# Optimization experiments

Measured on AMD Instinct MI355X. Metric: run time of the kernel, lower is better.

The kernel has to match this reference:

```python
import jax, jax.numpy as jnp
import numpy as np

D_MODEL = 512
N_HEADS = 8
D_K = D_MODEL // N_HEADS
WINDOW = 64
SCALE = 1.0 / np.sqrt(D_K)


def setup_inputs() -> dict:
    key = jax.random.key(0)
    ks = jax.random.split(key, 9)
    B, S = 1, 2048
    s = 1.0 / np.sqrt(D_MODEL)
    inp = {
        "x": jax.random.normal(ks[0], (B, S, D_MODEL), dtype=jnp.float32),
        "Wq": jax.random.normal(ks[1], (D_MODEL, D_MODEL), dtype=jnp.float32) * s,
        "bq": jnp.zeros((D_MODEL,), dtype=jnp.float32),
        "Wk": jax.random.normal(ks[2], (D_MODEL, D_MODEL), dtype=jnp.float32) * s,
        "bk": jnp.zeros((D_MODEL,), dtype=jnp.float32),
        "Wv": jax.random.normal(ks[3], (D_MODEL, D_MODEL), dtype=jnp.float32) * s,
        "bv": jnp.zeros((D_MODEL,), dtype=jnp.float32),
        "Wo": jax.random.normal(ks[4], (D_MODEL, D_MODEL), dtype=jnp.float32) * s,
        "bo": jnp.zeros((D_MODEL,), dtype=jnp.float32),
    }
    return inp


def reference(x, Wq, bq, Wk, bk, Wv, bv, Wo, bo):
    B, S, _ = x.shape
    # projections (torch Linear: x @ W.T + b); split heads -> [B,S,H,dk]
    q = (x @ Wq.T + bq).reshape(B, S, N_HEADS, D_K)
    k = (x @ Wk.T + bk).reshape(B, S, N_HEADS, D_K)
    v = (x @ Wv.T + bv).reshape(B, S, N_HEADS, D_K)

    # banded window indices: position i attends to [i-W, i+W]
    L = 2 * WINDOW + 1
    offsets = jnp.arange(L) - WINDOW                    # [L]
    pos = jnp.arange(S)[:, None] + offsets[None, :]     # [S, L]
    valid = (pos >= 0) & (pos < S)                      # [S, L]
    posc = jnp.clip(pos, 0, S - 1)

    k_w = k[:, posc]                                    # [B, S, L, H, dk]
    v_w = v[:, posc]                                    # [B, S, L, H, dk]

    scores = jnp.einsum("bshd,bslhd->bhsl", q, k_w) * SCALE
    scores = jnp.where(valid[None, None, :, :], scores, -jnp.inf)
    attn = jax.nn.softmax(scores, axis=-1)              # [B, H, S, L]
    out = jnp.einsum("bhsl,bslhd->bshd", attn, v_w)     # [B, S, H, dk]
    out = out.reshape(B, S, D_MODEL)
    return out @ Wo.T + bo
```

## Files before the change

kernel.cpp:

```cpp
#include <hip/hip_runtime.h>
#include <hip/hip_bf16.h>
#include <math.h>

#define S_LEN  2048
#define DMODEL 512
#define NHEADS 8
#define DK     64
#define WIN    64

static constexpr float SCALE = 0.125f;

typedef short bf16x8 __attribute__((ext_vector_type(8)));
typedef float f32x4  __attribute__((ext_vector_type(4)));

__device__ __forceinline__ short bfh(float v)
{
    __hip_bfloat16 b = __float2bfloat16(v);
    return *reinterpret_cast<short*>(&b);
}
__device__ __forceinline__ float bf2f(short s)
{
    __hip_bfloat16 b = *reinterpret_cast<__hip_bfloat16*>(&s);
    return __bfloat162float(b);
}
__device__ __forceinline__ void split1(float v, short& h, short& l)
{
    h = bfh(v);
    l = bfh(v - bf2f(h));
}
__device__ __forceinline__ void split8(const float4 a0, const float4 a1,
                                       bf16x8& h8, bf16x8& l8)
{
    short hh, ll;
    split1(a0.x, hh, ll); h8[0] = hh; l8[0] = ll;
    split1(a0.y, hh, ll); h8[1] = hh; l8[1] = ll;
    split1(a0.z, hh, ll); h8[2] = hh; l8[2] = ll;
    split1(a0.w, hh, ll); h8[3] = hh; l8[3] = ll;
    split1(a1.x, hh, ll); h8[4] = hh; l8[4] = ll;
    split1(a1.y, hh, ll); h8[5] = hh; l8[5] = ll;
    split1(a1.z, hh, ll); h8[6] = hh; l8[6] = ll;
    split1(a1.w, hh, ll); h8[7] = hh; l8[7] = ll;
}

__device__ __forceinline__ void dma16(const void* g, void* l)
{
    __builtin_amdgcn_global_load_lds(
        (const __attribute__((address_space(1))) unsigned int*)g,
        (__attribute__((address_space(3))) unsigned int*)l, 16, 0, 0);
}

__global__ __launch_bounds__(256)
void cast_w(const float* __restrict__ wq, const float* __restrict__ wk,
            const float* __restrict__ wv, const float* __restrict__ wo,
            short* __restrict__ wqb, short* __restrict__ wkb,
            short* __restrict__ wvb, short* __restrict__ wob)
{
    const float* s; short* d;
    switch (blockIdx.z) {
        case 0:  s = wq; d = wqb; break;
        case 1:  s = wk; d = wkb; break;
        case 2:  s = wv; d = wvb; break;
        default: s = wo; d = wob; break;
    }
    for (int i = blockIdx.x * 256 + threadIdx.x; i < 65536; i += gridDim.x * 256) {
        const float4 v = ((const float4*)s)[i];
        short4 o;
        o.x = bfh(v.x); o.y = bfh(v.y); o.z = bfh(v.z); o.w = bfh(v.w);
        ((short4*)d)[i] = o;
    }
}

__global__ __launch_bounds__(128)
void gemm_qkv4(const float* __restrict__ x,
               const short* __restrict__ wqb, const short* __restrict__ wkb,
               const short* __restrict__ wvb,
               const float* __restrict__ bq, const float* __restrict__ bk,
               const float* __restrict__ bv,
               short* __restrict__ qh, short* __restrict__ ql,
               short* __restrict__ kb, short* __restrict__ vbt)
{
    __shared__ __align__(16) short sB[64 * 256];

    const int z = blockIdx.z;
    const short* Bg   = (z == 0) ? wqb : (z == 1) ? wkb : wvb;
    const float* bias = (z == 0) ? bq  : (z == 1) ? bk  : bv;
    const int row0 = blockIdx.y * 64;
    const int col0 = blockIdx.x * 64;
    const int tid  = threadIdx.x;
    const int lane = tid & 63;
    const int wv   = tid >> 6;
    const int col  = lane & 15;
    const int quad = lane >> 4;

    f32x4 acc[2][4];
#pragma unroll
    for (int mi = 0; mi < 2; ++mi)
#pragma unroll
        for (int nj = 0; nj < 4; ++nj)
            acc[mi][nj] = (f32x4)0.0f;

    for (int ph = 0; ph < 2; ++ph) {
        __syncthreads();
        for (int i = wv; i < 32; i += 2) {
            const int q = i * 64 + lane;
            const int r = q >> 5;
            const int b = q & 31;
            const int j = b ^ (r & 7);
            dma16(Bg + (size_t)(col0 + r) * 512 + ph * 256 + j * 8, sB + i * 512);
        }
        __syncthreads();

#pragma unroll
        for (int kc = 0; kc < 8; ++kc) {
            const int k = ph * 256 + kc * 32;
            bf16x8 ah[2], al[2];
#pragma unroll
            for (int mi = 0; mi < 2; ++mi) {
                const int m = row0 + wv * 32 + mi * 16 + col;
                const float* xp = x + (size_t)m * 512 + k + quad * 8;
                const float4 a0 = *(const float4*)xp;
                const float4 a1 = *(const float4*)(xp + 4);
                split8(a0, a1, ah[mi], al[mi]);
            }
#pragma unroll
            for (int nj = 0; nj < 4; ++nj) {
                const int n = nj * 16 + col;
                const int j = (kc * 4 + quad) ^ (n & 7);
                const bf16x8 bf = *(const bf16x8*)&sB[n * 256 + j * 8];
#pragma unroll
                for (int mi = 0; mi < 2; ++mi) {
                    acc[mi][nj] = __builtin_amdgcn_mfma_f32_16x16x32_bf16(ah[mi], bf, acc[mi][nj], 0, 0, 0);
                    acc[mi][nj] = __builtin_amdgcn_mfma_f32_16x16x32_bf16(al[mi], bf, acc[mi][nj], 0, 0, 0);
                }
            }
        }
    }

#pragma unroll
    for (int nj = 0; nj < 4; ++nj) {
        const int cc = col0 + nj * 16 + col;
        const float bias_v = bias[cc];
#pragma unroll
        for (int mi = 0; mi < 2; ++mi) {
#pragma unroll
            for (int e = 0; e < 4; ++e) {
                const int row = row0 + wv * 32 + mi * 16 + quad * 4 + e;
                const float val = acc[mi][nj][e] + bias_v;
                if (z == 0) {
                    short hh, ll;
                    split1(val, hh, ll);
                    qh[(size_t)row * 512 + cc] = hh;
                    ql[(size_t)row * 512 + cc] = ll;
                } else if (z == 1) {
                    kb[(size_t)row * 512 + cc] = bfh(val);
                } else {
                    vbt[(size_t)cc * 2048 + row] = bfh(val);
                }
            }
        }
    }
}

__global__ __launch_bounds__(128)
void gemm_out4(const short* __restrict__ ah_g,
               const short* __restrict__ wob, const float* __restrict__ bo,
               float* __restrict__ out)
{
    __shared__ __align__(16) short sB[64 * 256];

    const int row0 = blockIdx.y * 32;
    const int col0 = blockIdx.x * 64;
    const int tid  = threadIdx.x;
    const int lane = tid & 63;
    const int wv   = tid >> 6;
    const int col  = lane & 15;
    const int quad = lane >> 4;

    f32x4 acc[4];
#pragma unroll
    for (int nj = 0; nj < 4; ++nj)
        acc[nj] = (f32x4)0.0f;

    for (int ph = 0; ph < 2; ++ph) {
        __syncthreads();
        for (int i = wv; i < 32; i += 2) {
            const int q = i * 64 + lane;
            const int r = q >> 5;
            const int b = q & 31;
            const int j = b ^ (r & 7);
            dma16(wob + (size_t)(col0 + r) * 512 + ph * 256 + j * 8, sB + i * 512);
        }
        __syncthreads();

#pragma unroll
        for (int kc = 0; kc < 8; ++kc) {
            const int k = ph * 256 + kc * 32;
            const int m = row0 + wv * 16 + col;
            const bf16x8 ah = *(const bf16x8*)(ah_g + (size_t)m * 512 + k + quad * 8);
#pragma unroll
            for (int nj = 0; nj < 4; ++nj) {
                const int n = nj * 16 + col;
                const int j = (kc * 4 + quad) ^ (n & 7);
                const bf16x8 bf = *(const bf16x8*)&sB[n * 256 + j * 8];
                acc[nj] = __builtin_amdgcn_mfma_f32_16x16x32_bf16(ah, bf, acc[nj], 0, 0, 0);
            }
        }
    }

#pragma unroll
    for (int nj = 0; nj < 4; ++nj) {
        const int cc = col0 + nj * 16 + col;
        const float bias_v = bo[cc];
#pragma unroll
        for (int e = 0; e < 4; ++e) {
            const int row = row0 + wv * 16 + quad * 4 + e;
            out[(size_t)row * 512 + cc] = acc[nj][e] + bias_v;
        }
    }
}

__global__ __launch_bounds__(256)
void banded_attn4(const short* __restrict__ qh, const short* __restrict__ ql,
                  const short* __restrict__ kb, const short* __restrict__ vbt,
                  short* __restrict__ abh)
{
    __shared__ __align__(16) short VtS[64 * 256];
    __shared__ __align__(16) short KS [192 * 64];
    __shared__ __align__(16) short QhS[32 * 64];
    __shared__ __align__(16) short QlS[32 * 64];
    __shared__ float pmax[4][32];
    __shared__ float psum[4][32];
    short* PS = KS;

    const int h    = blockIdx.x;
    const int t0   = blockIdx.y * 32;
    const int tid  = threadIdx.x;
    const int lane = tid & 63;
    const int wv   = tid >> 6;
    const int col  = lane & 15;
    const int quad = lane >> 4;

    {
        const int lr = lane >> 3;
        const int lc = lane & 7;
        for (int i = wv; i < 32; i += 4) {
            const short* src; short* dst; int r;
            if (i < 4) {
                r = i * 8 + lr;
                src = qh + (size_t)(t0 + r) * 512 + h * 64;
                dst = QhS + i * 512;
            } else if (i < 8) {
                const int g = i - 4;
                r = g * 8 + lr;
                src = ql + (size_t)(t0 + r) * 512 + h * 64;
                dst = QlS + g * 512;
            } else {
                const int g = i - 8;
                r = g * 8 + lr;
                int pos = t0 - 64 + r;
                pos = pos < 0 ? 0 : (pos > 2047 ? 2047 : pos);
                src = kb + (size_t)pos * 512 + h * 64;
                dst = KS + g * 512;
            }
            const int cs = lc ^ (r & 7);
            dma16(src + cs * 8, dst);
        }
        for (int i = wv; i < 32; i += 4) {
            const int q = i * 64 + lane;
            const int d = q >> 5;
            const int b = q & 31;
            const int j0 = (b < 24) ? b : 0;
            const int j = j0 ^ (d & 7);
            int p0 = t0 - 64 + j * 8;
            p0 = p0 < 0 ? 0 : (p0 > 2040 ? 2040 : p0);
            dma16(vbt + (size_t)(h * 64 + d) * 2048 + p0, VtS + i * 512);
        }
    }
    __syncthreads();

    f32x4 sacc[2][3];
#pragma unroll
    for (int mi = 0; mi < 2; ++mi)
#pragma unroll
        for (int nj = 0; nj < 3; ++nj)
            sacc[mi][nj] = (f32x4)0.0f;

#pragma unroll
    for (int ks = 0; ks < 2; ++ks) {
        const int q0 = ks * 4 + quad;
        bf16x8 aqh[2], aql[2];
#pragma unroll
        for (int mi = 0; mi < 2; ++mi) {
            const int m = mi * 16 + col;
            const int p = q0 ^ (m & 7);
            aqh[mi] = *(const bf16x8*)&QhS[m * 64 + p * 8];
            aql[mi] = *(const bf16x8*)&QlS[m * 64 + p * 8];
        }
#pragma unroll
        for (int nj = 0; nj < 3; ++nj) {
            const int n = wv * 48 + nj * 16 + col;
            const int p = q0 ^ (n & 7);
            const bf16x8 bkf = *(const bf16x8*)&KS[n * 64 + p * 8];
#pragma unroll
            for (int mi = 0; mi < 2; ++mi) {
                sacc[mi][nj] = __builtin_amdgcn_mfma_f32_16x16x32_bf16(aqh[mi], bkf, sacc[mi][nj], 0, 0, 0);
                sacc[mi][nj] = __builtin_amdgcn_mfma_f32_16x16x32_bf16(aql[mi], bkf, sacc[mi][nj], 0, 0, 0);
            }
        }
    }

    float pv[2][3][4];
#pragma unroll
    for (int mi = 0; mi < 2; ++mi)
#pragma unroll
        for (int nj = 0; nj < 3; ++nj)
#pragma unroll
            for (int e = 0; e < 4; ++e) {
                const int r32 = mi * 16 + quad * 4 + e;
                const int n   = wv * 48 + nj * 16 + col;
                const int pos = t0 - 64 + n;
                const int d   = n - r32;
                const bool valid = (pos >= 0) && (pos < S_LEN) && (d >= 0) && (d <= 128);
                pv[mi][nj][e] = valid ? sacc[mi][nj][e] * SCALE : -__builtin_inff();
            }

#pragma unroll
    for (int mi = 0; mi < 2; ++mi)
#pragma unroll
        for (int e = 0; e < 4; ++e) {
            float mx = fmaxf(fmaxf(pv[mi][0][e], pv[mi][1][e]), pv[mi][2][e]);
#pragma unroll
            for (int off = 1; off < 16; off <<= 1)
                mx = fmaxf(mx, __shfl_xor(mx, off));
            if ((lane & 15) == 0) pmax[wv][mi * 16 + quad * 4 + e] = mx;
        }
    __syncthreads();

#pragma unroll
    for (int mi = 0; mi < 2; ++mi)
#pragma unroll
        for (int e = 0; e < 4; ++e) {
            const int r32 = mi * 16 + quad * 4 + e;
            const float m = fmaxf(fmaxf(pmax[0][r32], pmax[1][r32]),
                                  fmaxf(pmax[2][r32], pmax[3][r32]));
            float ss = 0.f;
#pragma unroll
            for (int nj = 0; nj < 3; ++nj) {
                const float p = __expf(pv[mi][nj][e] - m);
                pv[mi][nj][e] = p;
                ss += p;
            }
#pragma unroll
            for (int off = 1; off < 16; off <<= 1)
                ss += __shfl_xor(ss, off);
            if ((lane & 15) == 0) psum[wv][r32] = ss;
#pragma unroll
            for (int nj = 0; nj < 3; ++nj) {
                const int n = wv * 48 + nj * 16 + col;
                PS[r32 * 200 + n] = bfh(pv[mi][nj][e]);
            }
        }
    __syncthreads();

    const int mi = wv >> 1;
    f32x4 oacc[2];
    oacc[0] = (f32x4)0.0f;
    oacc[1] = (f32x4)0.0f;
#pragma unroll
    for (int ks = 0; ks < 6; ++ks) {
        const bf16x8 pa = *(const bf16x8*)&PS[(mi * 16 + col) * 200 + ks * 32 + quad * 8];
#pragma unroll
        for (int t = 0; t < 2; ++t) {
            const int d = ((wv & 1) * 2 + t) * 16 + col;
            const int j = (ks * 4 + quad) ^ (d & 7);
            const bf16x8 vf = *(const bf16x8*)&VtS[d * 256 + j * 8];
            oacc[t] = __builtin_amdgcn_mfma_f32_16x16x32_bf16(pa, vf, oacc[t], 0, 0, 0);
        }
    }

    float linv[4];
#pragma unroll
    for (int e = 0; e < 4; ++e) {
        const int r32 = mi * 16 + quad * 4 + e;
        linv[e] = 1.0f / (psum[0][r32] + psum[1][r32] + psum[2][r32] + psum[3][r32]);
    }
#pragma unroll
    for (int t = 0; t < 2; ++t) {
        const int nj = (wv & 1) * 2 + t;
#pragma unroll
        for (int e = 0; e < 4; ++e) {
            const int r32 = mi * 16 + quad * 4 + e;
            const float val = oacc[t][e] * linv[e];
            const size_t idx = (size_t)(t0 + r32) * 512 + h * 64 + nj * 16 + col;
            abh[idx] = bfh(val);
        }
    }
}

extern "C" void kernel_launch(void* const* d_in, const int* in_sizes, int n_in,
                              void* d_out, int out_size, void* d_ws, size_t ws_size,
                              hipStream_t stream)
{
    const float* x  = (const float*)d_in[0];
    const float* Wq = (const float*)d_in[1];
    const float* bq = (const float*)d_in[2];
    const float* Wk = (const float*)d_in[3];
    const float* bk = (const float*)d_in[4];
    const float* Wv = (const float*)d_in[5];
    const float* bv = (const float*)d_in[6];
    const float* Wo = (const float*)d_in[7];
    const float* bo = (const float*)d_in[8];
    float* out = (float*)d_out;

    char* ws = (char*)d_ws;
    short* qh  = (short*)(ws);
    short* ql  = (short*)(ws + (2u << 20));
    short* kb  = (short*)(ws + (4u << 20));
    short* vbt = (short*)(ws + (6u << 20));
    short* abh = (short*)(ws + (8u << 20));
    short* wqb = (short*)(ws + (12u << 20));
    short* wkb = (short*)(ws + (12u << 20) + 1 * (512u << 10));
    short* wvb = (short*)(ws + (12u << 20) + 2 * (512u << 10));
    short* wob = (short*)(ws + (12u << 20) + 3 * (512u << 10));

    dim3 gw(64, 1, 4);
    cast_w<<<gw, 256, 0, stream>>>(Wq, Wk, Wv, Wo, wqb, wkb, wvb, wob);

    dim3 gq(DMODEL / 64, S_LEN / 64, 3);
    gemm_qkv4<<<gq, 128, 0, stream>>>(x, wqb, wkb, wvb,
                                      bq, bk, bv, qh, ql, kb, vbt);

    dim3 ga(NHEADS, S_LEN / 32);
    banded_attn4<<<ga, 256, 0, stream>>>(qh, ql, kb, vbt, abh);

    dim3 go(DMODEL / 64, S_LEN / 32);
    gemm_out4<<<go, 128, 0, stream>>>(abh, wob, bo, out);
}
```

Before: 112.5 us.

## Fuse weight bf16 conversion into projection GEMMs and drop cast kernel

Removes the separate weight-cast kernel and its extra launch. The QKV and output GEMMs now DMA fp32 weights into shared memory with an XOR swizzle and round them to bf16 in registers just before each MFMA. The QKV GEMM tile drops to 32 rows, doubling its block count, and the x hi/lo split uses a bit-trick rounding. In exchange each weight tile takes twice the LDS bytes per k-chunk and every block repeats the fp32-to-bf16 packing work.

```diff
diff --git a/kernel.cpp b/kernel.cpp
--- a/kernel.cpp
+++ b/kernel.cpp
@@ -28,18 +28,37 @@
     h = bfh(v);
     l = bfh(v - bf2f(h));
 }
-__device__ __forceinline__ void split8(const float4 a0, const float4 a1,
-                                       bf16x8& h8, bf16x8& l8)
-{
-    short hh, ll;
-    split1(a0.x, hh, ll); h8[0] = hh; l8[0] = ll;
-    split1(a0.y, hh, ll); h8[1] = hh; l8[1] = ll;
-    split1(a0.z, hh, ll); h8[2] = hh; l8[2] = ll;
-    split1(a0.w, hh, ll); h8[3] = hh; l8[3] = ll;
-    split1(a1.x, hh, ll); h8[4] = hh; l8[4] = ll;
-    split1(a1.y, hh, ll); h8[5] = hh; l8[5] = ll;
-    split1(a1.z, hh, ll); h8[6] = hh; l8[6] = ll;
-    split1(a1.w, hh, ll); h8[7] = hh; l8[7] = ll;
+
+__device__ __forceinline__ unsigned rhu2(float f0, float f1)
+{
+    unsigned b0, b1;
+    __builtin_memcpy(&b0, &f0, 4);
+    __builtin_memcpy(&b1, &f1, 4);
+    return ((b1 + 0x8000u) & 0xffff0000u) | ((b0 + 0x8000u) >> 16);
+}
+__device__ __forceinline__ bf16x8 packW(const float4 w0, const float4 w1)
+{
+    union { unsigned u[4]; bf16x8 v; } r;
+    r.u[0] = rhu2(w0.x, w0.y);
+    r.u[1] = rhu2(w0.z, w0.w);
+    r.u[2] = rhu2(w1.x, w1.y);
+    r.u[3] = rhu2(w1.z, w1.w);
+    return r.v;
+}
+__device__ __forceinline__ void splitx8(const float4 a0, const float4 a1,
+                                        bf16x8& h8, bf16x8& l8)
+{
+    float f[8] = {a0.x, a0.y, a0.z, a0.w, a1.x, a1.y, a1.z, a1.w};
+#pragma unroll
+    for (int i = 0; i < 8; ++i) {
+        unsigned b;
+        __builtin_memcpy(&b, &f[i], 4);
+        const unsigned hb = (b + 0x8000u) & 0xffff0000u;
+        h8[i] = (short)(hb >> 16);
+        float hf;
+        __builtin_memcpy(&hf, &hb, 4);
+        l8[i] = bfh(f[i] - hf);
+    }
 }
 
 __device__ __forceinline__ void dma16(const void* g, void* l)
@@ -49,125 +68,20 @@
         (__attribute__((address_space(3))) unsigned int*)l, 16, 0, 0);
 }
 
-__global__ __launch_bounds__(256)
-void cast_w(const float* __restrict__ wq, const float* __restrict__ wk,
-            const float* __restrict__ wv, const float* __restrict__ wo,
-            short* __restrict__ wqb, short* __restrict__ wkb,
-            short* __restrict__ wvb, short* __restrict__ wob)
-{
-    const float* s; short* d;
-    switch (blockIdx.z) {
-        case 0:  s = wq; d = wqb; break;
-        case 1:  s = wk; d = wkb; break;
-        case 2:  s = wv; d = wvb; break;
-        default: s = wo; d = wob; break;
-    }
-    for (int i = blockIdx.x * 256 + threadIdx.x; i < 65536; i += gridDim.x * 256) {
-        const float4 v = ((const float4*)s)[i];
-        short4 o;
-        o.x = bfh(v.x); o.y = bfh(v.y); o.z = bfh(v.z); o.w = bfh(v.w);
-        ((short4*)d)[i] = o;
-    }
-}
-
 __global__ __launch_bounds__(128)
-void gemm_qkv4(const float* __restrict__ x,
-               const short* __restrict__ wqb, const short* __restrict__ wkb,
-               const short* __restrict__ wvb,
+void gemm_qkv5(const float* __restrict__ x,
+               const float* __restrict__ Wqf, const float* __restrict__ Wkf,
+               const float* __restrict__ Wvf,
                const float* __restrict__ bq, const float* __restrict__ bk,
                const float* __restrict__ bv,
                short* __restrict__ qh, short* __restrict__ ql,
                short* __restrict__ kb, short* __restrict__ vbt)
 {
-    __shared__ __align__(16) short sB[64 * 256];
+    __shared__ __align__(16) float sW[64 * 128];
 
     const int z = blockIdx.z;
-    const short* Bg   = (z == 0) ? wqb : (z == 1) ? wkb : wvb;
+    const float* Wg   = (z == 0) ? Wqf : (z == 1) ? Wkf : Wvf;
     const float* bias = (z == 0) ? bq  : (z == 1) ? bk  : bv;
-    const int row0 = blockIdx.y * 64;
-    const int col0 = blockIdx.x * 64;
-    const int tid  = threadIdx.x;
-    const int lane = tid & 63;
-    const int wv   = tid >> 6;
-    const int col  = lane & 15;
-    const int quad = lane >> 4;
-
-    f32x4 acc[2][4];
-#pragma unroll
-    for (int mi = 0; mi < 2; ++mi)
-#pragma unroll
-        for (int nj = 0; nj < 4; ++nj)
-            acc[mi][nj] = (f32x4)0.0f;
-
-    for (int ph = 0; ph < 2; ++ph) {
-        __syncthreads();
-        for (int i = wv; i < 32; i += 2) {
-            const int q = i * 64 + lane;
-            const int r = q >> 5;
-            const int b = q & 31;
-            const int j = b ^ (r & 7);
-            dma16(Bg + (size_t)(col0 + r) * 512 + ph * 256 + j * 8, sB + i * 512);
-        }
-        __syncthreads();
-
-#pragma unroll
-        for (int kc = 0; kc < 8; ++kc) {
-            const int k = ph * 256 + kc * 32;
-            bf16x8 ah[2], al[2];
-#pragma unroll
-            for (int mi = 0; mi < 2; ++mi) {
-                const int m = row0 + wv * 32 + mi * 16 + col;
-                const float* xp = x + (size_t)m * 512 + k + quad * 8;
-                const float4 a0 = *(const float4*)xp;
-                const float4 a1 = *(const float4*)(xp + 4);
-                split8(a0, a1, ah[mi], al[mi]);
-            }
-#pragma unroll
-            for (int nj = 0; nj < 4; ++nj) {
-                const int n = nj * 16 + col;
-                const int j = (kc * 4 + quad) ^ (n & 7);
-                const bf16x8 bf = *(const bf16x8*)&sB[n * 256 + j * 8];
-#pragma unroll
-                for (int mi = 0; mi < 2; ++mi) {
-                    acc[mi][nj] = __builtin_amdgcn_mfma_f32_16x16x32_bf16(ah[mi], bf, acc[mi][nj], 0, 0, 0);
-                    acc[mi][nj] = __builtin_amdgcn_mfma_f32_16x16x32_bf16(al[mi], bf, acc[mi][nj], 0, 0, 0);
-                }
-            }
-        }
-    }
-
-#pragma unroll
-    for (int nj = 0; nj < 4; ++nj) {
-        const int cc = col0 + nj * 16 + col;
-        const float bias_v = bias[cc];
-#pragma unroll
-        for (int mi = 0; mi < 2; ++mi) {
-#pragma unroll
-            for (int e = 0; e < 4; ++e) {
-                const int row = row0 + wv * 32 + mi * 16 + quad * 4 + e;
-                const float val = acc[mi][nj][e] + bias_v;
-                if (z == 0) {
-                    short hh, ll;
-                    split1(val, hh, ll);
-                    qh[(size_t)row * 512 + cc] = hh;
-                    ql[(size_t)row * 512 + cc] = ll;
-                } else if (z == 1) {
-                    kb[(size_t)row * 512 + cc] = bfh(val);
-                } else {
-                    vbt[(size_t)cc * 2048 + row] = bfh(val);
-                }
-            }
-        }
-    }
-}
-
-__global__ __launch_bounds__(128)
-void gemm_out4(const short* __restrict__ ah_g,
-               const short* __restrict__ wob, const float* __restrict__ bo,
-               float* __restrict__ out)
-{
-    __shared__ __align__(16) short sB[64 * 256];
-
     const int row0 = blockIdx.y * 32;
     const int col0 = blockIdx.x * 64;
     const int tid  = threadIdx.x;
@@ -175,34 +89,111 @@
     const int wv   = tid >> 6;
     const int col  = lane & 15;
     const int quad = lane >> 4;
+    const int m    = row0 + wv * 16 + col;
 
     f32x4 acc[4];
 #pragma unroll
     for (int nj = 0; nj < 4; ++nj)
         acc[nj] = (f32x4)0.0f;
 
-    for (int ph = 0; ph < 2; ++ph) {
+    for (int ph = 0; ph < 4; ++ph) {
         __syncthreads();
         for (int i = wv; i < 32; i += 2) {
-            const int q = i * 64 + lane;
-            const int r = q >> 5;
-            const int b = q & 31;
-            const int j = b ^ (r & 7);
-            dma16(wob + (size_t)(col0 + r) * 512 + ph * 256 + j * 8, sB + i * 512);
+            const int r = 2 * i + (lane >> 5);
+            const int c = lane & 31;
+            const int j = c ^ (r & 7);
+            dma16(Wg + (size_t)(col0 + r) * 512 + ph * 128 + j * 4, sW + i * 256);
         }
         __syncthreads();
 
 #pragma unroll
-        for (int kc = 0; kc < 8; ++kc) {
-            const int k = ph * 256 + kc * 32;
-            const int m = row0 + wv * 16 + col;
-            const bf16x8 ah = *(const bf16x8*)(ah_g + (size_t)m * 512 + k + quad * 8);
+        for (int kc = 0; kc < 4; ++kc) {
+            const int k = ph * 128 + kc * 32;
+            const float* xp = x + (size_t)m * 512 + k + quad * 8;
+            const float4 a0 = *(const float4*)xp;
+            const float4 a1 = *(const float4*)(xp + 4);
+            bf16x8 ah, al;
+            splitx8(a0, a1, ah, al);
 #pragma unroll
             for (int nj = 0; nj < 4; ++nj) {
-                const int n = nj * 16 + col;
-                const int j = (kc * 4 + quad) ^ (n & 7);
-                const bf16x8 bf = *(const bf16x8*)&sB[n * 256 + j * 8];
-                acc[nj] = __builtin_amdgcn_mfma_f32_16x16x32_bf16(ah, bf, acc[nj], 0, 0, 0);
+                const int n  = nj * 16 + col;
+                const int s  = n & 7;
+                const int c0 = kc * 8 + quad * 2;
+                const float4 w0 = *(const float4*)&sW[n * 128 + ((c0    ) ^ s) * 4];
+                const float4 w1 = *(const float4*)&sW[n * 128 + ((c0 + 1) ^ s) * 4];
+                const bf16x8 wf = packW(w0, w1);
+                acc[nj] = __builtin_amdgcn_mfma_f32_16x16x32_bf16(ah, wf, acc[nj], 0, 0, 0);
+                acc[nj] = __builtin_amdgcn_mfma_f32_16x16x32_bf16(al, wf, acc[nj], 0, 0, 0);
+            }
+        }
+    }
+
+#pragma unroll
+    for (int nj = 0; nj < 4; ++nj) {
+        const int cc = col0 + nj * 16 + col;
+        const float bias_v = bias[cc];
+#pragma unroll
+        for (int e = 0; e < 4; ++e) {
+            const int row = row0 + wv * 16 + quad * 4 + e;
+            const float val = acc[nj][e] + bias_v;
+            if (z == 0) {
+                short hh, ll;
+                split1(val, hh, ll);
+                qh[(size_t)row * 512 + cc] = hh;
+                ql[(size_t)row * 512 + cc] = ll;
+            } else if (z == 1) {
+                kb[(size_t)row * 512 + cc] = bfh(val);
+            } else {
+                vbt[(size_t)cc * 2048 + row] = bfh(val);
+            }
+        }
+    }
+}
+
+__global__ __launch_bounds__(128)
+void gemm_out5(const short* __restrict__ ah_g,
+               const float* __restrict__ Wof, const float* __restrict__ bo,
+               float* __restrict__ out)
+{
+    __shared__ __align__(16) float sW[64 * 128];
+
+    const int row0 = blockIdx.y * 32;
+    const int col0 = blockIdx.x * 64;
+    const int tid  = threadIdx.x;
+    const int lane = tid & 63;
+    const int wv   = tid >> 6;
+    const int col  = lane & 15;
+    const int quad = lane >> 4;
+    const int m    = row0 + wv * 16 + col;
+
+    f32x4 acc[4];
+#pragma unroll
+    for (int nj = 0; nj < 4; ++nj)
+        acc[nj] = (f32x4)0.0f;
+
+    for (int ph = 0; ph < 4; ++ph) {
+        __syncthreads();
+        for (int i = wv; i < 32; i += 2) {
+            const int r = 2 * i + (lane >> 5);
+            const int c = lane & 31;
+            const int j = c ^ (r & 7);
+            dma16(Wof + (size_t)(col0 + r) * 512 + ph * 128 + j * 4, sW + i * 256);
+        }
+        __syncthreads();
+
+#pragma unroll
+        for (int kc = 0; kc < 4; ++kc) {
+            const int k = ph * 128 + kc * 32;
+            const bf16x8 af = *(const bf16x8*)(ah_g + (size_t)m * 512 + k + quad * 8);
+#pragma unroll
+            for (int nj = 0; nj < 4; ++nj) {
+                const int n  = nj * 16 + col;
+                const int s  = n & 7;
+                const int c0 = kc * 8 + quad * 2;
+                const float4 w0 = *(const float4*)&sW[n * 128 + ((c0    ) ^ s) * 4];
+                const float4 w1 = *(const float4*)&sW[n * 128 + ((c0 + 1) ^ s) * 4];
+                const bf16x8 wf = packW(w0, w1);
+                acc[nj] = __builtin_amdgcn_mfma_f32_16x16x32_bf16(af, wf, acc[nj], 0, 0, 0);
             }
         }
     }
@@ -418,21 +409,14 @@
     short* kb  = (short*)(ws + (4u << 20));
     short* vbt = (short*)(ws + (6u << 20));
     short* abh = (short*)(ws + (8u << 20));
-    short* wqb = (short*)(ws + (12u << 20));
-    short* wkb = (short*)(ws + (12u << 20) + 1 * (512u << 10));
-    short* wvb = (short*)(ws + (12u << 20) + 2 * (512u << 10));
-    short* wob = (short*)(ws + (12u << 20) + 3 * (512u << 10));
-
-    dim3 gw(64, 1, 4);
-    cast_w<<<gw, 256, 0, stream>>>(Wq, Wk, Wv, Wo, wqb, wkb, wvb, wob);
-
-    dim3 gq(DMODEL / 64, S_LEN / 64, 3);
-    gemm_qkv4<<<gq, 128, 0, stream>>>(x, wqb, wkb, wvb,
+
+    dim3 gq(DMODEL / 64, S_LEN / 32, 3);
+    gemm_qkv5<<<gq, 128, 0, stream>>>(x, Wq, Wk, Wv,
                                       bq, bk, bv, qh, ql, kb, vbt);
 
     dim3 ga(NHEADS, S_LEN / 32);
     banded_attn4<<<ga, 256, 0, stream>>>(qh, ql, kb, vbt, abh);
 
     dim3 go(DMODEL / 64, S_LEN / 32);
-    gemm_out4<<<go, 128, 0, stream>>>(abh, wob, bo, out);
-}
+    gemm_out5<<<go, 128, 0, stream>>>(abh, Wo, bo, out);
+}
```

New measurement: 128.0 us. 1.14x slower.

## Drop LDS staging and read MFMA operands directly from global memory

Applied to the files above, without the earlier changes.

Removes the global_load_lds DMA staging of weight tiles, Q/K/V tiles and the accompanying barriers from the QKV GEMM, the output GEMM and the banded attention kernel. Each MFMA operand is now loaded straight from global memory, relying on L1/L2 caching instead of shared-memory reuse. The QKV GEMM switches to 256 threads, with each wave owning 16 rows instead of 32. This cuts LDS traffic and synchronisation but repeats global loads of the same weight and K/V data across waves, which may strain cache bandwidth.

```diff
diff --git a/kernel.cpp b/kernel.cpp
--- a/kernel.cpp
+++ b/kernel.cpp
@@ -28,25 +28,17 @@
     h = bfh(v);
     l = bfh(v - bf2f(h));
 }
-__device__ __forceinline__ void split8(const float4 a0, const float4 a1,
-                                       bf16x8& h8, bf16x8& l8)
-{
-    short hh, ll;
-    split1(a0.x, hh, ll); h8[0] = hh; l8[0] = ll;
-    split1(a0.y, hh, ll); h8[1] = hh; l8[1] = ll;
-    split1(a0.z, hh, ll); h8[2] = hh; l8[2] = ll;
-    split1(a0.w, hh, ll); h8[3] = hh; l8[3] = ll;
-    split1(a1.x, hh, ll); h8[4] = hh; l8[4] = ll;
-    split1(a1.y, hh, ll); h8[5] = hh; l8[5] = ll;
-    split1(a1.z, hh, ll); h8[6] = hh; l8[6] = ll;
-    split1(a1.w, hh, ll); h8[7] = hh; l8[7] = ll;
-}
-
-__device__ __forceinline__ void dma16(const void* g, void* l)
-{
-    __builtin_amdgcn_global_load_lds(
-        (const __attribute__((address_space(1))) unsigned int*)g,
-        (__attribute__((address_space(3))) unsigned int*)l, 16, 0, 0);
+__device__ __forceinline__ void splitx8(const float4 a0, const float4 a1,
+                                        bf16x8& h8, bf16x8& l8)
+{
+    float f[8] = {a0.x, a0.y, a0.z, a0.w, a1.x, a1.y, a1.z, a1.w};
+#pragma unroll
+    for (int i = 0; i < 8; ++i) {
+        short hh, ll;
+        split1(f[i], hh, ll);
+        h8[i] = hh;
+        l8[i] = ll;
+    }
 }
 
 __global__ __launch_bounds__(256)
@@ -70,8 +62,8 @@
     }
 }
 
-__global__ __launch_bounds__(128)
-void gemm_qkv4(const float* __restrict__ x,
+__global__ __launch_bounds__(256)
+void gemm_qkv6(const float* __restrict__ x,
                const short* __restrict__ wqb, const short* __restrict__ wkb,
                const short* __restrict__ wvb,
                const float* __restrict__ bq, const float* __restrict__ bk,
@@ -79,8 +71,6 @@
                short* __restrict__ qh, short* __restrict__ ql,
                short* __restrict__ kb, short* __restrict__ vbt)
 {
-    __shared__ __align__(16) short sB[64 * 256];
-
     const int z = blockIdx.z;
     const short* Bg   = (z == 0) ? wqb : (z == 1) ? wkb : wvb;
     const float* bias = (z == 0) ? bq  : (z == 1) ? bk  : bv;
@@ -91,48 +81,26 @@
     const int wv   = tid >> 6;
     const int col  = lane & 15;
     const int quad = lane >> 4;
-
-    f32x4 acc[2][4];
-#pragma unroll
-    for (int mi = 0; mi < 2; ++mi)
-#pragma unroll
-        for (int nj = 0; nj < 4; ++nj)
-            acc[mi][nj] = (f32x4)0.0f;
-
-    for (int ph = 0; ph < 2; ++ph) {
-        __syncthreads();
-        for (int i = wv; i < 32; i += 2) {
-            const int q = i * 64 + lane;
-            const int r = q >> 5;
-            const int b = q & 31;
-            const int j = b ^ (r & 7);
-            dma16(Bg + (size_t)(col0 + r) * 512 + ph * 256 + j * 8, sB + i * 512);
-        }
-        __syncthreads();
-
-#pragma unroll
-        for (int kc = 0; kc < 8; ++kc) {
-            const int k = ph * 256 + kc * 32;
-            bf16x8 ah[2], al[2];
-#pragma unroll
-            for (int mi = 0; mi < 2; ++mi) {
-                const int m = row0 + wv * 32 + mi * 16 + col;
-                const float* xp = x + (size_t)m * 512 + k + quad * 8;
-                const float4 a0 = *(const float4*)xp;
-                const float4 a1 = *(const float4*)(xp + 4);
-                split8(a0, a1, ah[mi], al[mi]);
-            }
-#pragma unroll
-            for (int nj = 0; nj < 4; ++nj) {
-                const int n = nj * 16 + col;
-                const int j = (kc * 4 + quad) ^ (n & 7);
-                const bf16x8 bf = *(const bf16x8*)&sB[n * 256 + j * 8];
-#pragma unroll
-                for (int mi = 0; mi < 2; ++mi) {
-                    acc[mi][nj] = __builtin_amdgcn_mfma_f32_16x16x32_bf16(ah[mi], bf, acc[mi][nj], 0, 0, 0);
-                    acc[mi][nj] = __builtin_amdgcn_mfma_f32_16x16x32_bf16(al[mi], bf, acc[mi][nj], 0, 0, 0);
-                }
-            }
+    const int m    = row0 + wv * 16 + col;
+
+    f32x4 acc[4];
+#pragma unroll
+    for (int nj = 0; nj < 4; ++nj)
+        acc[nj] = (f32x4)0.0f;
+
+#pragma unroll 4
+    for (int kc = 0; kc < 16; ++kc) {
+        const float* xp = x + (size_t)m * 512 + kc * 32 + quad * 8;
+        const float4 a0 = *(const float4*)xp;
+        const float4 a1 = *(const float4*)(xp + 4);
+        bf16x8 ah, al;
+        splitx8(a0, a1, ah, al);
+#pragma unroll
+        for (int nj = 0; nj < 4; ++nj) {
+            const int n = col0 + nj * 16 + col;
+            const bf16x8 bf = *(const bf16x8*)(Bg + (size_t)n * 512 + kc * 32 + quad * 8);
+            acc[nj] = __builtin_amdgcn_mfma_f32_16x16x32_bf16(ah, bf, acc[nj], 0, 0, 0);
+            acc[nj] = __builtin_amdgcn_mfma_f32_16x16x32_bf16(al, bf, acc[nj], 0, 0, 0);
         }
     }
 
@@ -141,33 +109,28 @@
         const int cc = col0 + nj * 16 + col;
         const float bias_v = bias[cc];
 #pragma unroll
-        for (int mi = 0; mi < 2; ++mi) {
-#pragma unroll
-            for (int e = 0; e < 4; ++e) {
-                const int row = row0 + wv * 32 + mi * 16 + quad * 4 + e;
-                const float val = acc[mi][nj][e] + bias_v;
-                if (z == 0) {
-                    short hh, ll;
-                    split1(val, hh, ll);
-                    qh[(size_t)row * 512 + cc] = hh;
-                    ql[(size_t)row * 512 + cc] = ll;
-                } else if (z == 1) {
-                    kb[(size_t)row * 512 + cc] = bfh(val);
-                } else {
-                    vbt[(size_t)cc * 2048 + row] = bfh(val);
-                }
+        for (int e = 0; e < 4; ++e) {
+            const int row = row0 + wv * 16 + quad * 4 + e;
+            const float val = acc[nj][e] + bias_v;
+            if (z == 0) {
+                short hh, ll;
+                split1(val, hh, ll);
+                qh[(size_t)row * 512 + cc] = hh;
+                ql[(size_t)row * 512 + cc] = ll;
+            } else if (z == 1) {
+                kb[(size_t)row * 512 + cc] = bfh(val);
+            } else {
+                vbt[(size_t)cc * 2048 + row] = bfh(val);
             }
         }
     }
 }
 
 __global__ __launch_bounds__(128)
-void gemm_out4(const short* __restrict__ ah_g,
+void gemm_out6(const short* __restrict__ ah_g,
                const short* __restrict__ wob, const float* __restrict__ bo,
                float* __restrict__ out)
 {
-    __shared__ __align__(16) short sB[64 * 256];
-
     const int row0 = blockIdx.y * 32;
     const int col0 = blockIdx.x * 64;
     const int tid  = threadIdx.x;
@@ -175,35 +138,21 @@
     const int wv   = tid >> 6;
     const int col  = lane & 15;
     const int quad = lane >> 4;
+    const int m    = row0 + wv * 16 + col;
 
     f32x4 acc[4];
 #pragma unroll
     for (int nj = 0; nj < 4; ++nj)
         acc[nj] = (f32x4)0.0f;
 
-    for (int ph = 0; ph < 2; ++ph) {
-        __syncthreads();
-        for (int i = wv; i < 32; i += 2) {
-            const int q = i * 64 + lane;
-            const int r = q >> 5;
-            const int b = q & 31;
-            const int j = b ^ (r & 7);
-            dma16(wob + (size_t)(col0 + r) * 512 + ph * 256 + j * 8, sB + i * 512);
-        }
-        __syncthreads();
-
-#pragma unroll
-        for (int kc = 0; kc < 8; ++kc) {
-            const int k = ph * 256 + kc * 32;
-            const int m = row0 + wv * 16 + col;
-            const bf16x8 ah = *(const bf16x8*)(ah_g + (size_t)m * 512 + k + quad * 8);
-#pragma unroll
-            for (int nj = 0; nj < 4; ++nj) {
-                const int n = nj * 16 + col;
-                const int j = (kc * 4 + quad) ^ (n & 7);
-                const bf16x8 bf = *(const bf16x8*)&sB[n * 256 + j * 8];
-                acc[nj] = __builtin_amdgcn_mfma_f32_16x16x32_bf16(ah, bf, acc[nj], 0, 0, 0);
-            }
+#pragma unroll
+    for (int kc = 0; kc < 16; ++kc) {
+        const bf16x8 af = *(const bf16x8*)(ah_g + (size_t)m * 512 + kc * 32 + quad * 8);
+#pragma unroll
+        for (int nj = 0; nj < 4; ++nj) {
+            const int n = col0 + nj * 16 + col;
+            const bf16x8 bf = *(const bf16x8*)(wob + (size_t)n * 512 + kc * 32 + quad * 8);
+            acc[nj] = __builtin_amdgcn_mfma_f32_16x16x32_bf16(af, bf, acc[nj], 0, 0, 0);
         }
     }
 
@@ -220,17 +169,13 @@
 }
 
 __global__ __launch_bounds__(256)
-void banded_attn4(const short* __restrict__ qh, const short* __restrict__ ql,
+void banded_attn5(const short* __restrict__ qh, const short* __restrict__ ql,
                   const short* __restrict__ kb, const short* __restrict__ vbt,
                   short* __restrict__ abh)
 {
-    __shared__ __align__(16) short VtS[64 * 256];
-    __shared__ __align__(16) short KS [192 * 64];
-    __shared__ __align__(16) short QhS[32 * 64];
-    __shared__ __align__(16) short QlS[32 * 64];
+    __shared__ __align__(16) short PS[32 * 200];
     __shared__ float pmax[4][32];
     __shared__ float psum[4][32];
-    short* PS = KS;
 
     const int h    = blockIdx.x;
     const int t0   = blockIdx.y * 32;
@@ -240,44 +185,6 @@
     const int col  = lane & 15;
     const int quad = lane >> 4;
 
-    {
-        const int lr = lane >> 3;
-        const int lc = lane & 7;
-        for (int i = wv; i < 32; i += 4) {
-            const short* src; short* dst; int r;
-            if (i < 4) {
-                r = i * 8 + lr;
-                src = qh + (size_t)(t0 + r) * 512 + h * 64;
-                dst = QhS + i * 512;
-            } else if (i < 8) {
-                const int g = i - 4;
-                r = g * 8 + lr;
-                src = ql + (size_t)(t0 + r) * 512 + h * 64;
-                dst = QlS + g * 512;
-            } else {
-                const int g = i - 8;
-                r = g * 8 + lr;
-                int pos = t0 - 64 + r;
-                pos = pos < 0 ? 0 : (pos > 2047 ? 2047 : pos);
-                src = kb + (size_t)pos * 512 + h * 64;
-                dst = KS + g * 512;
-            }
-            const int cs = lc ^ (r & 7);
-            dma16(src + cs * 8, dst);
-        }
-        for (int i = wv; i < 32; i += 4) {
-            const int q = i * 64 + lane;
-            const int d = q >> 5;
-            const int b = q & 31;
-            const int j0 = (b < 24) ? b : 0;
-            const int j = j0 ^ (d & 7);
-            int p0 = t0 - 64 + j * 8;
-            p0 = p0 < 0 ? 0 : (p0 > 2040 ? 2040 : p0);
-            dma16(vbt + (size_t)(h * 64 + d) * 2048 + p0, VtS + i * 512);
-        }
-    }
-    __syncthreads();
-
     f32x4 sacc[2][3];
 #pragma unroll
     for (int mi = 0; mi < 2; ++mi)
@@ -287,20 +194,19 @@
 
 #pragma unroll
     for (int ks = 0; ks < 2; ++ks) {
-        const int q0 = ks * 4 + quad;
         bf16x8 aqh[2], aql[2];
 #pragma unroll
         for (int mi = 0; mi < 2; ++mi) {
-            const int m = mi * 16 + col;
-            const int p = q0 ^ (m & 7);
-            aqh[mi] = *(const bf16x8*)&QhS[m * 64 + p * 8];
-            aql[mi] = *(const bf16x8*)&QlS[m * 64 + p * 8];
+            const size_t qoff = (size_t)(t0 + mi * 16 + col) * 512 + h * 64 + ks * 32 + quad * 8;
+            aqh[mi] = *(const bf16x8*)(qh + qoff);
+            aql[mi] = *(const bf16x8*)(ql + qoff);
         }
 #pragma unroll
         for (int nj = 0; nj < 3; ++nj) {
             const int n = wv * 48 + nj * 16 + col;
-            const int p = q0 ^ (n & 7);
-            const bf16x8 bkf = *(const bf16x8*)&KS[n * 64 + p * 8];
+            int pos = t0 - 64 + n;
+            pos = pos < 0 ? 0 : (pos > 2047 ? 2047 : pos);
+            const bf16x8 bkf = *(const bf16x8*)(kb + (size_t)pos * 512 + h * 64 + ks * 32 + quad * 8);
 #pragma unroll
             for (int mi = 0; mi < 2; ++mi) {
                 sacc[mi][nj] = __builtin_amdgcn_mfma_f32_16x16x32_bf16(aqh[mi], bkf, sacc[mi][nj], 0, 0, 0);
@@ -369,11 +275,12 @@
 #pragma unroll
     for (int ks = 0; ks < 6; ++ks) {
         const bf16x8 pa = *(const bf16x8*)&PS[(mi * 16 + col) * 200 + ks * 32 + quad * 8];
+        int wpos = t0 - 64 + ks * 32 + quad * 8;
+        wpos = wpos < 0 ? 0 : (wpos > 2040 ? 2040 : wpos);
 #pragma unroll
         for (int t = 0; t < 2; ++t) {
             const int d = ((wv & 1) * 2 + t) * 16 + col;
-            const int j = (ks * 4 + quad) ^ (d & 7);
-            const bf16x8 vf = *(const bf16x8*)&VtS[d * 256 + j * 8];
+            const bf16x8 vf = *(const bf16x8*)(vbt + (size_t)(h * 64 + d) * 2048 + wpos);
             oacc[t] = __builtin_amdgcn_mfma_f32_16x16x32_bf16(pa, vf, oacc[t], 0, 0, 0);
         }
     }
@@ -427,12 +334,12 @@
     cast_w<<<gw, 256, 0, stream>>>(Wq, Wk, Wv, Wo, wqb, wkb, wvb, wob);
 
     dim3 gq(DMODEL / 64, S_LEN / 64, 3);
-    gemm_qkv4<<<gq, 128, 0, stream>>>(x, wqb, wkb, wvb,
+    gemm_qkv6<<<gq, 256, 0, stream>>>(x, wqb, wkb, wvb,
                                       bq, bk, bv, qh, ql, kb, vbt);
 
     dim3 ga(NHEADS, S_LEN / 32);
-    banded_attn4<<<ga, 256, 0, stream>>>(qh, ql, kb, vbt, abh);
+    banded_attn5<<<ga, 256, 0, stream>>>(qh, ql, kb, vbt, abh);
 
     dim3 go(DMODEL / 64, S_LEN / 32);
-    gemm_out4<<<go, 128, 0, stream>>>(abh, wob, bo, out);
-}
+    gemm_out6<<<go, 128, 0, stream>>>(abh, wob, bo, out);
+}
```

After: 135.0 us. 20.0% more time.
